# Kernel optimization log

Measured on AMD Instinct MI355X. Metric: run time of the kernel, lower is better.

The kernel has to match this reference:

```python
import jax, jax.numpy as jnp
import numpy as np

ALPHA = 0.2      # LeakyReLU negative slope
DROPOUT_P = 0.1  # torch F.dropout default training=True, so it IS applied
D_OUT = 128


def setup_inputs() -> dict:
    key = jax.random.key(0)
    k1, k2, k3 = jax.random.split(key, 3)
    N, D_IN = 8192, 128
    batch = jax.random.normal(k1, (N, D_IN), dtype=jnp.float32)
    # xavier_uniform gain=1.414 scale for faithfulness of magnitude
    w = jax.random.uniform(k2, (D_IN, D_OUT), dtype=jnp.float32, minval=-1.0, maxval=1.0) * (1.414 * np.sqrt(6.0 / (D_IN + D_OUT)))
    a = jax.random.uniform(k3, (2 * D_OUT, 1), dtype=jnp.float32, minval=-1.0, maxval=1.0) * (1.414 * np.sqrt(6.0 / (2 * D_OUT + 1)))
    return {"batch": batch, "w": w, "a": a}


def reference(batch, w, a):
    h = batch.reshape(-1, w.shape[0])            # [N, D_in]
    Wh = h @ w                                   # [N, D_out]
    Wh1 = Wh @ a[:D_OUT, :]                      # [N, 1]
    Wh2 = Wh @ a[D_OUT:, :]                      # [N, 1]
    e = Wh1 + Wh2.T                              # [N, N] additive scores
    e = jnp.where(e > 0, e, ALPHA * e)           # LeakyReLU
    attention = jax.nn.softmax(e, axis=1)        # row softmax
    # dropout with a fixed key (deterministic reference)
    keep = jax.random.bernoulli(jax.random.key(42), 1.0 - DROPOUT_P, attention.shape)
    attention = jnp.where(keep, attention / (1.0 - DROPOUT_P), 0.0)
    h_prime = attention @ Wh                     # [N, D_out]
    return jax.nn.elu(h_prime)                   # concat=True -> elu
```

## Files before the change

kernel.cpp:

```cpp
#include <hip/hip_runtime.h>
#include <stdint.h>

#define ALPHA 0.2f

typedef __bf16 bf16x8 __attribute__((ext_vector_type(8)));
typedef float f32x4 __attribute__((ext_vector_type(4)));

__device__ __forceinline__ uint32_t rotl32(uint32_t x, int r) {
  return __builtin_amdgcn_alignbit(x, x, 32 - r);
}

__device__ __forceinline__ uint32_t tf_mix(uint32_t f) {
  const uint32_t ks1 = 42u, ks2 = 0x1BD11BF0u;
  uint32_t x0 = 0u;
  uint32_t x1 = f + ks1;
#define TFR(r) { x0 += x1; x1 = rotl32(x1, r); x1 ^= x0; }
  TFR(13) TFR(15) TFR(26) TFR(6)  x0 += ks1; x1 += ks2 + 1u;
  TFR(17) TFR(29) TFR(16) TFR(24) x0 += ks2; x1 += 0u  + 2u;
  TFR(13) TFR(15) TFR(26) TFR(6)  x0 += 0u;  x1 += ks1 + 3u;
  TFR(17) TFR(29) TFR(16) TFR(24) x0 += ks1; x1 += ks2 + 4u;
  TFR(13) TFR(15) TFR(26) TFR(6)  x0 += ks2; x1 += 0u  + 5u;
#undef TFR
  return x0 ^ x1;
}

__device__ __forceinline__ unsigned short f2bf(float f) {
  uint32_t u = __float_as_uint(f);
  return (unsigned short)((u + 0x7fffu + ((u >> 16) & 1u)) >> 16);
}

__global__ __launch_bounds__(256) void wh_kernel(
    const float* __restrict__ batch, const float* __restrict__ w,
    const float* __restrict__ a, unsigned short* __restrict__ WhbT,
    float* __restrict__ s1, float* __restrict__ s2, uint32_t* __restrict__ s2key) {
  __shared__ float whlds[32][128];
  int t = threadIdx.x;
  int i0 = blockIdx.x * 32;
  int d = t & 127, rg = t >> 7;
  int ib = i0 + rg * 16;
  float acc[16];
#pragma unroll
  for (int r = 0; r < 16; ++r) acc[r] = 0.f;
  for (int k = 0; k < 128; k += 4) {
    float wv0 = w[(k + 0) * 128 + d];
    float wv1 = w[(k + 1) * 128 + d];
    float wv2 = w[(k + 2) * 128 + d];
    float wv3 = w[(k + 3) * 128 + d];
#pragma unroll
    for (int r = 0; r < 16; ++r) {
      float4 b4 = *(const float4*)&batch[(ib + r) * 128 + k];
      acc[r] = fmaf(b4.w, wv3, fmaf(b4.z, wv2, fmaf(b4.y, wv1, fmaf(b4.x, wv0, acc[r]))));
    }
  }
  unsigned short hb[16];
#pragma unroll
  for (int r = 0; r < 16; ++r) {
    whlds[rg * 16 + r][d] = acc[r];
    hb[r] = f2bf(acc[r]);
  }
  uint32_t pk[8];
#pragma unroll
  for (int q = 0; q < 8; ++q) pk[q] = (uint32_t)hb[2 * q] | ((uint32_t)hb[2 * q + 1] << 16);
  uint4* dst = (uint4*)&WhbT[d * 8192 + ib];
  dst[0] = make_uint4(pk[0], pk[1], pk[2], pk[3]);
  dst[1] = make_uint4(pk[4], pk[5], pk[6], pk[7]);
  __syncthreads();
  int rr = t >> 3, seg = t & 7, c0 = seg * 16;
  const float* wr = &whlds[rr][c0];
  float p1 = 0.f, p2 = 0.f;
#pragma unroll
  for (int c = 0; c < 16; ++c) {
    float v = wr[c];
    p1 = fmaf(v, a[c0 + c], p1);
    p2 = fmaf(v, a[128 + c0 + c], p2);
  }
  p1 += __shfl_xor(p1, 1, 64); p1 += __shfl_xor(p1, 2, 64); p1 += __shfl_xor(p1, 4, 64);
  p2 += __shfl_xor(p2, 1, 64); p2 += __shfl_xor(p2, 2, 64); p2 += __shfl_xor(p2, 4, 64);
  if (seg == 0) { s1[i0 + rr] = p1; s2[i0 + rr] = p2; }
  float v = (seg == 0) ? p2 : -3.4e38f;
#pragma unroll
  for (int m = 1; m <= 32; m <<= 1) v = fmaxf(v, __shfl_xor(v, m, 64));
  if ((t & 63) == 0) {
    uint32_t b = __float_as_uint(v);
    uint32_t key = (b & 0x80000000u) ? ~b : (b | 0x80000000u);
    atomicMax(s2key, key);
  }
}

__global__ __launch_bounds__(512, 8) void gat_main(
    const float* __restrict__ s1, const float* __restrict__ s2g,
    const uint32_t* __restrict__ s2key, const unsigned short* __restrict__ WhbT,
    float* __restrict__ pacc, float* __restrict__ pz) {
  __shared__ __align__(16) float s2c[4096];
  __shared__ __align__(16) unsigned short plds[16 * 64];
  int t = threadIdx.x;
  int rb = blockIdx.x >> 1, ck = blockIdx.x & 1;
  int R0 = rb * 16, C0 = ck * 4096;

  for (int k = t; k < 1024; k += 512)
    ((float4*)s2c)[k] = ((const float4*)(s2g + C0))[k];

  uint32_t kk = *s2key;
  uint32_t mb = (kk & 0x80000000u) ? (kk ^ 0x80000000u) : ~kk;
  float s2max = __uint_as_float(mb);

  int r = t >> 5, jt = t & 31;
  float s1r = s1[R0 + r];
  float xm = s1r + s2max;
  float mr = fmaxf(xm, ALPHA * xm);
  float z = 0.f;
  uint32_t cbase = (uint32_t)(R0 + r) * 8192u + (uint32_t)(C0 + 2 * jt);
  int j0loc = 2 * jt;
  int pw = r * 64 + ((((j0loc >> 3)) ^ (r & 7)) << 3) + (j0loc & 7);

  int w = t >> 6, lane = t & 63;
  int arow = lane & 15, g = lane >> 4;
  int aoff0 = arow * 64 + ((g ^ (arow & 7)) << 3);
  int aoff1 = arow * 64 + (((g + 4) ^ (arow & 7)) << 3);
  const unsigned short* bbase = WhbT + (w * 16 + (lane & 15)) * 8192 + C0 + g * 8;
  f32x4 acc = {0.f, 0.f, 0.f, 0.f};
  const uint32_t KTH = 0xE6666600u;

  __syncthreads();

  for (int jb = 0; jb < 4096; jb += 64) {
    bf16x8 B0 = *(const bf16x8*)(bbase + jb);
    bf16x8 B1 = *(const bf16x8*)(bbase + jb + 32);
    float sj0 = s2c[jb + j0loc], sj1 = s2c[jb + j0loc + 1];
    uint32_t c = cbase + (uint32_t)jb;
    uint32_t b0 = tf_mix(c), b1 = tf_mix(c + 1u);
    float x0 = s1r + sj0; float e0 = fmaxf(x0, ALPHA * x0); float p0 = __expf(e0 - mr);
    float x1 = s1r + sj1; float e1 = fmaxf(x1, ALPHA * x1); float p1 = __expf(e1 - mr);
    z += p0 + p1;
    uint32_t pk = (uint32_t)f2bf(b0 < KTH ? p0 : 0.f) |
                  ((uint32_t)f2bf(b1 < KTH ? p1 : 0.f) << 16);
    *(uint32_t*)&plds[pw] = pk;
    __syncthreads();
    bf16x8 A0 = *(const bf16x8*)&plds[aoff0];
    bf16x8 A1 = *(const bf16x8*)&plds[aoff1];
    acc = __builtin_amdgcn_mfma_f32_16x16x32_bf16(A0, B0, acc, 0, 0, 0);
    acc = __builtin_amdgcn_mfma_f32_16x16x32_bf16(A1, B1, acc, 0, 0, 0);
    __syncthreads();
  }

#pragma unroll
  for (int m = 1; m <= 16; m <<= 1) z += __shfl_xor(z, m, 64);
  if (jt == 0) atomicAdd(&pz[R0 + r], z);

  int dcol = w * 16 + (lane & 15);
#pragma unroll
  for (int reg = 0; reg < 4; ++reg) {
    int row = (lane >> 4) * 4 + reg;
    atomicAdd(&pacc[(R0 + row) * 128 + dcol], acc[reg]);
  }
}

__global__ __launch_bounds__(256) void gat_final(
    const float* __restrict__ pacc, const float* __restrict__ pz,
    float* __restrict__ out) {
  int t = threadIdx.x;
  int row = blockIdx.x * 8 + (t >> 5);
  int d4 = (t & 31) * 4;
  float zinv = 1.f / (0.9f * pz[row]);
  float4 p = *(const float4*)&pacc[row * 128 + d4];
  float4 o;
  float v;
  v = p.x * zinv; o.x = v > 0.f ? v : expm1f(v);
  v = p.y * zinv; o.y = v > 0.f ? v : expm1f(v);
  v = p.z * zinv; o.z = v > 0.f ? v : expm1f(v);
  v = p.w * zinv; o.w = v > 0.f ? v : expm1f(v);
  *(float4*)&out[row * 128 + d4] = o;
}

extern "C" void kernel_launch(void* const* d_in, const int* in_sizes, int n_in,
                              void* d_out, int out_size, void* d_ws, size_t ws_size,
                              hipStream_t stream) {
  const float* batch = (const float*)d_in[0];
  const float* w = (const float*)d_in[1];
  const float* a = (const float*)d_in[2];
  float* out = (float*)d_out;
  char* ws = (char*)d_ws;
  float* pacc = (float*)ws;
  float* pz = (float*)(ws + 4194304);
  uint32_t* s2key = (uint32_t*)(ws + 4194304 + 32768);
  unsigned short* WhbT = (unsigned short*)(ws + 4194304 + 32768 + 64);
  float* s1 = (float*)(ws + 4194304 + 32768 + 64 + 2097152);
  float* s2 = (float*)(ws + 4194304 + 32768 + 64 + 2097152 + 32768);

  hipMemsetAsync(ws, 0, 4194304 + 32768 + 64, stream);
  wh_kernel<<<256, 256, 0, stream>>>(batch, w, a, WhbT, s1, s2, s2key);
  gat_main<<<1024, 512, 0, stream>>>(s1, s2, s2key, WhbT, pacc, pz);
  gat_final<<<1024, 256, 0, stream>>>(pacc, pz, out);
}
```

Before: 214.0 us.

## Restructure attention kernel so each lane computes its own MFMA A-fragment, removing LDS round-trip

The Wh matrix is now stored in a blocked layout matching MFMA B-fragments. Each wave computes probabilities directly in the A-operand register layout, so the shared-memory staging and two barriers per iteration go away. Each wave now reuses one A fragment across 8 output tiles, and the four waves' partial sums are combined in LDS before the atomics. The exp is folded into exp2 with prescaled scores, and block size drops to 256 threads. In exchange there is more register pressure from 8 accumulators and 8 B vectors, plus an extra cross-wave reduction.

```diff
diff --git a/kernel.cpp b/kernel.cpp
--- a/kernel.cpp
+++ b/kernel.cpp
@@ -2,9 +2,11 @@
 #include <stdint.h>
 
 #define ALPHA 0.2f
+#define LOG2E 1.4426950408889634f
 
 typedef __bf16 bf16x8 __attribute__((ext_vector_type(8)));
 typedef float f32x4 __attribute__((ext_vector_type(4)));
+typedef uint32_t u32x4 __attribute__((ext_vector_type(4)));
 
 __device__ __forceinline__ uint32_t rotl32(uint32_t x, int r) {
   return __builtin_amdgcn_alignbit(x, x, 32 - r);
@@ -31,7 +33,7 @@
 
 __global__ __launch_bounds__(256) void wh_kernel(
     const float* __restrict__ batch, const float* __restrict__ w,
-    const float* __restrict__ a, unsigned short* __restrict__ WhbT,
+    const float* __restrict__ a, unsigned short* __restrict__ whb2,
     float* __restrict__ s1, float* __restrict__ s2, uint32_t* __restrict__ s2key) {
   __shared__ float whlds[32][128];
   int t = threadIdx.x;
@@ -61,9 +63,9 @@
   uint32_t pk[8];
 #pragma unroll
   for (int q = 0; q < 8; ++q) pk[q] = (uint32_t)hb[2 * q] | ((uint32_t)hb[2 * q + 1] << 16);
-  uint4* dst = (uint4*)&WhbT[d * 8192 + ib];
-  dst[0] = make_uint4(pk[0], pk[1], pk[2], pk[3]);
-  dst[1] = make_uint4(pk[4], pk[5], pk[6], pk[7]);
+  uint32_t base0 = (((uint32_t)(ib >> 3) * 16u + (uint32_t)(d & 15)) * 8u + (uint32_t)(d >> 4)) * 8u;
+  *(uint4*)&whb2[base0]        = make_uint4(pk[0], pk[1], pk[2], pk[3]);
+  *(uint4*)&whb2[base0 + 1024] = make_uint4(pk[4], pk[5], pk[6], pk[7]);
   __syncthreads();
   int rr = t >> 3, seg = t & 7, c0 = seg * 16;
   const float* wr = &whlds[rr][c0];
@@ -87,71 +89,101 @@
   }
 }
 
-__global__ __launch_bounds__(512, 8) void gat_main(
+__global__ __launch_bounds__(256, 4) void gat_main(
     const float* __restrict__ s1, const float* __restrict__ s2g,
-    const uint32_t* __restrict__ s2key, const unsigned short* __restrict__ WhbT,
+    const uint32_t* __restrict__ s2key, const unsigned short* __restrict__ whb2,
     float* __restrict__ pacc, float* __restrict__ pz) {
-  __shared__ __align__(16) float s2c[4096];
-  __shared__ __align__(16) unsigned short plds[16 * 64];
+  __shared__ __align__(16) float smem[8256];
   int t = threadIdx.x;
   int rb = blockIdx.x >> 1, ck = blockIdx.x & 1;
   int R0 = rb * 16, C0 = ck * 4096;
 
-  for (int k = t; k < 1024; k += 512)
-    ((float4*)s2c)[k] = ((const float4*)(s2g + C0))[k];
+  for (int k = t; k < 1024; k += 256) {
+    float4 v4 = ((const float4*)(s2g + C0))[k];
+    v4.x *= LOG2E; v4.y *= LOG2E; v4.z *= LOG2E; v4.w *= LOG2E;
+    ((float4*)smem)[k] = v4;
+  }
 
   uint32_t kk = *s2key;
   uint32_t mb = (kk & 0x80000000u) ? (kk ^ 0x80000000u) : ~kk;
-  float s2max = __uint_as_float(mb);
-
-  int r = t >> 5, jt = t & 31;
-  float s1r = s1[R0 + r];
-  float xm = s1r + s2max;
-  float mr = fmaxf(xm, ALPHA * xm);
+  float s2maxL = __uint_as_float(mb) * LOG2E;
+
+  int w = t >> 6, lane = t & 63;
+  int r = lane & 15, q = lane >> 4;
+
+  float s1L = s1[R0 + r] * LOG2E;
+  float xmL = s1L + s2maxL;
+  float mrL = fmaxf(xmL, ALPHA * xmL);
+  float Ar = s1L - mrL;
+  float Cr = (ALPHA - 1.f) * mrL;
+
+  uint32_t fb = (uint32_t)(R0 + r) * 8192u + (uint32_t)(C0 + w * 32 + q * 8);
+  uint32_t voff = (((uint32_t)(C0 / 8 + w * 4 + q)) * 16u + (uint32_t)r) * 128u;
+  const char* pB = (const char*)whb2;
+
+  f32x4 acc[8];
+#pragma unroll
+  for (int dt = 0; dt < 8; ++dt) acc[dt] = (f32x4){0.f, 0.f, 0.f, 0.f};
   float z = 0.f;
-  uint32_t cbase = (uint32_t)(R0 + r) * 8192u + (uint32_t)(C0 + 2 * jt);
-  int j0loc = 2 * jt;
-  int pw = r * 64 + ((((j0loc >> 3)) ^ (r & 7)) << 3) + (j0loc & 7);
-
-  int w = t >> 6, lane = t & 63;
-  int arow = lane & 15, g = lane >> 4;
-  int aoff0 = arow * 64 + ((g ^ (arow & 7)) << 3);
-  int aoff1 = arow * 64 + (((g + 4) ^ (arow & 7)) << 3);
-  const unsigned short* bbase = WhbT + (w * 16 + (lane & 15)) * 8192 + C0 + g * 8;
-  f32x4 acc = {0.f, 0.f, 0.f, 0.f};
   const uint32_t KTH = 0xE6666600u;
-
-  __syncthreads();
-
-  for (int jb = 0; jb < 4096; jb += 64) {
-    bf16x8 B0 = *(const bf16x8*)(bbase + jb);
-    bf16x8 B1 = *(const bf16x8*)(bbase + jb + 32);
-    float sj0 = s2c[jb + j0loc], sj1 = s2c[jb + j0loc + 1];
-    uint32_t c = cbase + (uint32_t)jb;
-    uint32_t b0 = tf_mix(c), b1 = tf_mix(c + 1u);
-    float x0 = s1r + sj0; float e0 = fmaxf(x0, ALPHA * x0); float p0 = __expf(e0 - mr);
-    float x1 = s1r + sj1; float e1 = fmaxf(x1, ALPHA * x1); float p1 = __expf(e1 - mr);
-    z += p0 + p1;
-    uint32_t pk = (uint32_t)f2bf(b0 < KTH ? p0 : 0.f) |
-                  ((uint32_t)f2bf(b1 < KTH ? p1 : 0.f) << 16);
-    *(uint32_t*)&plds[pw] = pk;
-    __syncthreads();
-    bf16x8 A0 = *(const bf16x8*)&plds[aoff0];
-    bf16x8 A1 = *(const bf16x8*)&plds[aoff1];
-    acc = __builtin_amdgcn_mfma_f32_16x16x32_bf16(A0, B0, acc, 0, 0, 0);
-    acc = __builtin_amdgcn_mfma_f32_16x16x32_bf16(A1, B1, acc, 0, 0, 0);
-    __syncthreads();
-  }
-
-#pragma unroll
-  for (int m = 1; m <= 16; m <<= 1) z += __shfl_xor(z, m, 64);
-  if (jt == 0) atomicAdd(&pz[R0 + r], z);
-
-  int dcol = w * 16 + (lane & 15);
-#pragma unroll
-  for (int reg = 0; reg < 4; ++reg) {
-    int row = (lane >> 4) * 4 + reg;
-    atomicAdd(&pacc[(R0 + row) * 128 + dcol], acc[reg]);
+  const float* sjb = smem + w * 32 + q * 8;
+
+  __syncthreads();
+
+  for (int it = 0; it < 32; ++it) {
+    bf16x8 Bv[8];
+#pragma unroll
+    for (int dt = 0; dt < 8; ++dt)
+      Bv[dt] = *(const bf16x8*)(pB + (voff + (uint32_t)(dt * 16)));
+    float4 sj0 = *(const float4*)(sjb + it * 128);
+    float4 sj1 = *(const float4*)(sjb + it * 128 + 4);
+    uint32_t f0 = fb + (uint32_t)(it * 128);
+
+    float p[8];
+    {
+      float sv[8] = {sj0.x, sj0.y, sj0.z, sj0.w, sj1.x, sj1.y, sj1.z, sj1.w};
+#pragma unroll
+      for (int s = 0; s < 8; ++s) {
+        uint32_t bits = tf_mix(f0 + (uint32_t)s);
+        float u = Ar + sv[s];
+        float arg = fmaxf(u, fmaf(ALPHA, u, Cr));
+        float pv = __builtin_amdgcn_exp2f(arg);
+        z += pv;
+        p[s] = (bits < KTH) ? pv : 0.f;
+      }
+    }
+    bf16x8 A;
+#pragma unroll
+    for (int s = 0; s < 8; ++s) A[s] = (__bf16)p[s];
+
+#pragma unroll
+    for (int dt = 0; dt < 8; ++dt)
+      acc[dt] = __builtin_amdgcn_mfma_f32_16x16x32_bf16(A, Bv[dt], acc[dt], 0, 0, 0);
+
+    voff += 32768u;
+  }
+
+  __syncthreads();
+  float zq = z + __shfl_xor(z, 16, 64);
+  zq += __shfl_xor(zq, 32, 64);
+  if (lane < 16) smem[8192 + w * 16 + lane] = zq;
+  float* red = smem;
+#pragma unroll
+  for (int dt = 0; dt < 8; ++dt) {
+#pragma unroll
+    for (int reg = 0; reg < 4; ++reg)
+      red[w * 2048 + (4 * q + reg) * 128 + dt * 16 + r] = acc[dt][reg];
+  }
+  __syncthreads();
+#pragma unroll
+  for (int k2 = 0; k2 < 8; ++k2) {
+    int idx = t * 8 + k2;
+    float s = (red[idx] + red[2048 + idx]) + (red[4096 + idx] + red[6144 + idx]);
+    atomicAdd(&pacc[(R0 + (idx >> 7)) * 128 + (idx & 127)], s);
+  }
+  if (t < 16) {
+    float zs = (smem[8192 + t] + smem[8208 + t]) + (smem[8224 + t] + smem[8240 + t]);
+    atomicAdd(&pz[R0 + t], zs);
   }
 }
 
@@ -183,12 +215,12 @@
   float* pacc = (float*)ws;
   float* pz = (float*)(ws + 4194304);
   uint32_t* s2key = (uint32_t*)(ws + 4194304 + 32768);
-  unsigned short* WhbT = (unsigned short*)(ws + 4194304 + 32768 + 64);
+  unsigned short* whb2 = (unsigned short*)(ws + 4194304 + 32768 + 64);
   float* s1 = (float*)(ws + 4194304 + 32768 + 64 + 2097152);
   float* s2 = (float*)(ws + 4194304 + 32768 + 64 + 2097152 + 32768);
 
   hipMemsetAsync(ws, 0, 4194304 + 32768 + 64, stream);
-  wh_kernel<<<256, 256, 0, stream>>>(batch, w, a, WhbT, s1, s2, s2key);
-  gat_main<<<1024, 512, 0, stream>>>(s1, s2, s2key, WhbT, pacc, pz);
+  wh_kernel<<<256, 256, 0, stream>>>(batch, w, a, whb2, s1, s2, s2key);
+  gat_main<<<1024, 256, 0, stream>>>(s1, s2, s2key, whb2, pacc, pz);
   gat_final<<<1024, 256, 0, stream>>>(pacc, pz, out);
 }
```

After: 233.4 us. 9.1% more time.
